# Optimization experiments

Hardware: AMD Instinct MI355X
Metric: run time of the kernel (lower is better)

## Reference

```python
import jax, jax.numpy as jnp
import numpy as np

B, C, H, W = 4, 128, 128, 128
NCLS = 80
NCONV = 2


def conv3x3(x, w, b):
    # x: [B,Cin,H,W], w: [Cout,Cin,3,3]
    y = jax.lax.conv_general_dilated(x, w, (1, 1), 'SAME',
                                     dimension_numbers=('NCHW', 'OIHW', 'NCHW'))
    return y + b[None, :, None, None]


def setup_inputs() -> dict:
    key = jax.random.key(0)
    ks = jax.random.split(key, 10)
    std = 0.01  # conv init std in the torch module
    prior_prob = 0.01
    bias_value = -np.log((1 - prior_prob) / prior_prob)
    inp = {
        'feature': jax.random.normal(ks[0], (B, C, H, W), jnp.float32),
        'targets': jax.random.uniform(ks[1], (B, NCLS, H, W), jnp.float32),
        'cls_w': std * jax.random.normal(ks[2], (NCONV, C, C, 3, 3), jnp.float32),
        'cls_b': jnp.zeros((NCONV, C), jnp.float32),
        'bbox_w': std * jax.random.normal(ks[3], (NCONV, C, C, 3, 3), jnp.float32),
        'bbox_b': jnp.zeros((NCONV, C), jnp.float32),
        'off_w': std * jax.random.normal(ks[4], (NCONV, C, C, 3, 3), jnp.float32),
        'off_b': jnp.zeros((NCONV, C), jnp.float32),
        'cls_score_w': std * jax.random.normal(ks[5], (NCLS, C, 3, 3), jnp.float32),
        'cls_score_b': jnp.full((NCLS,), bias_value, jnp.float32),
        'bbox_pred_w': std * jax.random.normal(ks[6], (2, C, 3, 3), jnp.float32),
        'bbox_pred_b': jnp.zeros((2,), jnp.float32),
        'center_off_w': std * jax.random.normal(ks[7], (2, C, 3, 3), jnp.float32),
        'center_off_b': jnp.zeros((2,), jnp.float32),
        'K': 100,
    }
    return inp


def centernet_forward(feature, targets, cls_w, cls_b, bbox_w, bbox_b, off_w, off_b,
                      cls_score_w, cls_score_b, bbox_pred_w, bbox_pred_b,
                      center_off_w, center_off_b, K):
    # ---- head: three conv+ReLU subnets + final 3x3 heads ----
    xc, xb, xo = feature, feature, feature
    for i in range(NCONV):
        xc = jax.nn.relu(conv3x3(xc, cls_w[i], cls_b[i]))
        xb = jax.nn.relu(conv3x3(xb, bbox_w[i], bbox_b[i]))
        xo = jax.nn.relu(conv3x3(xo, off_w[i], off_b[i]))
    logits = conv3x3(xc, cls_score_w, cls_score_b)      # [B,NCLS,H,W]
    wh = conv3x3(xb, bbox_pred_w, bbox_pred_b)          # [B,2,H,W]
    off = conv3x3(xo, center_off_w, center_off_b)       # [B,2,H,W]

    # ---- center focal loss (alpha=2, beta=4, reduction='sum') ----
    pos = (targets == 1.0).astype(logits.dtype)
    neg = (targets < 1.0).astype(logits.dtype)
    neg_w = jnp.power(1.0 - targets, 4.0)
    p = jax.nn.sigmoid(logits)
    log_p = jax.nn.log_sigmoid(logits)        # log(sigmoid(x))
    log_1mp = jax.nn.log_sigmoid(-logits)     # log(1 - sigmoid(x))
    pos_loss = log_p * jnp.square(1.0 - p) * pos
    neg_loss = log_1mp * jnp.square(p) * neg_w * neg
    loss = -(pos_loss.sum()) - (neg_loss.sum())

    # ---- decode: sigmoid + 3x3 maxpool pseudo-NMS + top-k + gather ----
    hm = p  # sigmoid heatmap
    hmax = jax.lax.reduce_window(hm, -jnp.inf, jax.lax.max,
                                 (1, 1, 3, 3), (1, 1, 1, 1), 'SAME')
    hm_nms = jnp.where(hmax == hm, hm, 0.0)
    scores, inds = jax.lax.top_k(hm_nms.reshape(B, -1), K)  # [B,K]
    hw = H * W
    clses = inds // hw                 # [B,K] int class ids
    sp = inds % hw                     # spatial index
    ys = (sp // W).astype(jnp.float32)
    xs = (sp % W).astype(jnp.float32)
    # gather wh/offset at peak locations
    wh_k = jnp.take_along_axis(wh.reshape(B, 2, hw), sp[:, None, :], axis=2)    # [B,2,K]
    off_k = jnp.take_along_axis(off.reshape(B, 2, hw), sp[:, None, :], axis=2)  # [B,2,K]
    cx = xs + off_k[:, 0]
    cy = ys + off_k[:, 1]
    w_, h_ = wh_k[:, 0], wh_k[:, 1]
    boxes = jnp.stack([cx - w_ / 2, cy - h_ / 2, cx + w_ / 2, cy + h_ / 2], axis=-1)  # [B,K,4]
    return boxes, scores, clses, loss


def reference(feature, targets, cls_w, cls_b, bbox_w, bbox_b, off_w, off_b,
              cls_score_w, cls_score_b, bbox_pred_w, bbox_pred_b,
              center_off_w, center_off_b, K):
    return centernet_forward(feature, targets, cls_w, cls_b, bbox_w, bbox_b,
                             off_w, off_b, cls_score_w, cls_score_b,
                             bbox_pred_w, bbox_pred_b, center_off_w,
                             center_off_b, K)
```

## Files before the change

### kernel.cpp

```cpp
#include <hip/hip_runtime.h>
#include <hip/hip_bf16.h>
#include <math.h>

#define B_    4
#define C_    128
#define H_    128
#define W_    128
#define HW_   (H_*W_)
#define NCLS_ 80
#define KTOP  100
#define CAPB  2048

typedef __attribute__((ext_vector_type(8)))  short bf16x8;
typedef __attribute__((ext_vector_type(16))) float f32x16;

#define WSTAGE_B   18432
#define WIMG_B     663552
#define NIMG       7
#define XROWB      144
#define XCOLS      130
#define XPITCH     (XCOLS * XROWB)
#define XSZ        ((size_t)16 * 130 * XPITCH)
#define XLDS_B     25920
#define LDS_TOT    (XLDS_B + 2 * WSTAGE_B)
#define ZERO_N     20512

__device__ __forceinline__ unsigned bf16_rne(float x) {
    unsigned u = __float_as_uint(x);
    return (u + 0x7FFFu + ((u >> 16) & 1u)) >> 16;
}
__device__ __forceinline__ void split2(float v0, float v1, unsigned& hiP, unsigned& loP) {
    unsigned h0 = bf16_rne(v0), h1 = bf16_rne(v1);
    float r0 = v0 - __uint_as_float(h0 << 16);
    float r1 = v1 - __uint_as_float(h1 << 16);
    unsigned l0 = bf16_rne(r0), l1 = bf16_rne(r1);
    hiP = h0 | (h1 << 16);
    loP = l0 | (l1 << 16);
}

#define MFMA32(a, bvec, c) __builtin_amdgcn_mfma_f32_32x32x16_bf16(a, bvec, c, 0, 0, 0)

__global__ __launch_bounds__(256) void init_k(char* __restrict__ xa, char* __restrict__ xb,
                                              unsigned* __restrict__ sm, float* __restrict__ loss)
{
    const int i = blockIdx.x * 256 + threadIdx.x;
    if (i < 16512) {
        char* buf = (i < 8256) ? xa : xb;
        const int j = (i < 8256) ? i : i - 8256;
        int R, col;
        if (j < 4160) {
            const int g = j / 260, rr = j % 260;
            R = g * 130 + ((rr < 130) ? 0 : 129);
            col = rr % 130;
        } else {
            const int q = j - 4160;
            const int g = q / 256, m = q % 256;
            R = g * 130 + 1 + (m >> 1);
            col = (m & 1) ? 129 : 0;
        }
        char* p = buf + ((size_t)R * XCOLS + col) * XROWB;
        #pragma unroll
        for (int k = 0; k < 9; k++) *(uint4*)(p + k * 16) = make_uint4(0, 0, 0, 0);
    } else {
        const int k = i - 16512;
        if (k < ZERO_N) sm[k] = 0u;
        if (k == ZERO_N) *loss = 0.f;
    }
}

struct WtArgs { const float* src[NIMG]; int cout[NIMG]; };

__global__ __launch_bounds__(256) void wtx_k(WtArgs a, unsigned short* wt)
{
    const int img = blockIdx.z;
    const int idx = blockIdx.x * 256 + threadIdx.x;
    const int cp    = idx & 15;
    const int co    = (idx >> 4) & 127;
    const int st    = idx >> 11;
    if (st >= 36) return;
    const int tap   = st % 9;
    const int chunk = st / 9;
    const float* w = a.src[img];
    const int Cout = a.cout[img];
    const int ci = chunk * 32 + 2 * cp;
    float v0 = 0.f, v1 = 0.f;
    if (co < Cout) {
        v0 = w[((size_t)co * 128 + ci) * 9 + tap];
        v1 = w[((size_t)co * 128 + ci + 1) * 9 + tap];
    }
    unsigned hiP, loP; split2(v0, v1, hiP, loP);
    char* dst = (char*)wt + (size_t)img * WIMG_B + ((size_t)st * 128 + co) * 144;
    *(unsigned*)(dst + 4 * cp)      = hiP;
    *(unsigned*)(dst + 64 + 4 * cp) = loP;
    if (cp < 4) *(unsigned*)(dst + 128 + 4 * cp) = 0u;
}

__device__ __forceinline__ void stage_w(const unsigned short* wt, char* lds,
                                        int s, int buf, int wv, int lane)
{
    const int nc    = (wv < 2) ? 5 : 4;
    const int start = (wv < 2) ? wv * 5 : 10 + (wv - 2) * 4;
    const char* src = (const char*)wt + (size_t)s * WSTAGE_B;
    char* dst = lds + XLDS_B + buf * WSTAGE_B;
    for (int i = 0; i < nc; i++) {
        const int off = (start + i) * 1024;
        __builtin_amdgcn_global_load_lds(
            (const __attribute__((address_space(1))) unsigned*)(src + off + lane * 16),
            (__attribute__((address_space(3))) unsigned*)(dst + off),
            16, 0, 0);
    }
}

template<int RELU, int XOUT>
__device__ __forceinline__ void conv_epilogue(
    f32x16 (&acc)[2][2], const bool* act,
    const float* bias, float* outf, char* outx, int Cout,
    int b, int x0, int y0, int wm, int wn, int kh, int l31)
{
    #pragma unroll
    for (int f = 0; f < 2; f++) {
        if (!act[f]) continue;
        if (XOUT == 0) {
            #pragma unroll
            for (int r = 0; r < 16; r++) {
                const int co = wm * 64 + f * 32 + 4 * kh + (r & 3) + 8 * (r >> 2);
                if (co < Cout) {
                    const float bv = bias[co];
                    #pragma unroll
                    for (int fn = 0; fn < 2; fn++) {
                        const int p = wn * 64 + fn * 32 + l31;
                        float v = acc[f][fn][r] + bv;
                        if (RELU) v = fmaxf(v, 0.f);
                        outf[((size_t)b * Cout + co) * HW_ + (size_t)(y0 + (p >> 4)) * 128 + (x0 + (p & 15))] = v;
                    }
                }
            }
        } else {
            const int chunkO = wm * 2 + f;
            #pragma unroll
            for (int r2 = 0; r2 < 8; r2++) {
                const int r = 2 * r2;
                const int cij = 4 * kh + (r & 3) + 8 * (r >> 2);
                const int co0 = wm * 64 + f * 32 + cij;
                const float b0v = bias[co0], b1v = bias[co0 + 1];
                #pragma unroll
                for (int fn = 0; fn < 2; fn++) {
                    const int p = wn * 64 + fn * 32 + l31;
                    float v0 = acc[f][fn][r] + b0v;
                    float v1 = acc[f][fn][r + 1] + b1v;
                    if (RELU) { v0 = fmaxf(v0, 0.f); v1 = fmaxf(v1, 0.f); }
                    unsigned hiP, loP; split2(v0, v1, hiP, loP);
                    char* rowp = outx + ((size_t)((b * 4 + chunkO) * 130 + (y0 + (p >> 4) + 1)) * XCOLS
                                        + (x0 + (p & 15) + 1)) * XROWB;
                    *(unsigned*)(rowp + 2 * cij)      = hiP;
                    *(unsigned*)(rowp + 64 + 2 * cij) = loP;
                }
            }
        }
    }
}

template<int RELU, int XOUT>
__global__ __launch_bounds__(256, 2) void conv_f_k(
    const float* __restrict__ in, const unsigned short* __restrict__ wt,
    const float* __restrict__ bias, float* __restrict__ outf,
    char* __restrict__ outx, int Cout)
{
    __shared__ __align__(16) char lds[LDS_TOT];

    const int t    = threadIdx.x;
    const int lane = t & 63;
    const int wv   = t >> 6;
    const int wm   = wv >> 1;
    const int wn   = wv & 1;
    const int l31  = lane & 31;
    const int kh   = lane >> 5;

    const int bi = blockIdx.x;
    const int x0 = (bi & 7) << 4;
    const int y0 = ((bi >> 3) & 15) << 3;
    const int b  = bi >> 7;

    int baddr[2];
    #pragma unroll
    for (int fn = 0; fn < 2; fn++) {
        const int p = wn * 64 + fn * 32 + l31;
        baddr[fn] = ((p >> 4) * 18 + (p & 15)) * 144 + kh * 16;
    }
    int aaddr[2];
    bool act[2];
    #pragma unroll
    for (int f = 0; f < 2; f++) {
        aaddr[f] = XLDS_B + (wm * 64 + f * 32 + l31) * 144 + kh * 16;
        act[f] = (wm * 64 + f * 32) < Cout;
    }

    f32x16 acc[2][2];
    #pragma unroll
    for (int i = 0; i < 2; i++)
        #pragma unroll
        for (int j = 0; j < 2; j++)
            #pragma unroll
            for (int r = 0; r < 16; r++) acc[i][j][r] = 0.f;

    const float* inb = in + (size_t)b * 128 * HW_;

    float xa[12], xb[12];
    #define LOADX(ch) do {                                                    \
        _Pragma("unroll")                                                     \
        for (int it = 0; it < 12; it++) {                                     \
            const int idx = t + it * 256;                                     \
            const int pl = idx & 15, cp = (idx >> 4) & 15, ph = idx >> 8;     \
            const int pos = ph * 16 + pl;                                     \
            float v0 = 0.f, v1 = 0.f;                                         \
            if (pos < 180) {                                                  \
                const int hy = pos / 18, hx = pos - hy * 18;                  \
                const int gy = y0 - 1 + hy, gx = x0 - 1 + hx;                 \
                if ((unsigned)gy < 128u && (unsigned)gx < 128u) {             \
                    const float* p0 = inb + (size_t)((ch) * 32 + 2 * cp) * HW_ \
                                          + gy * 128 + gx;                    \
                    v0 = p0[0]; v1 = p0[HW_];                                 \
                }                                                             \
            }                                                                 \
            xa[it] = v0; xb[it] = v1;                                         \
        }                                                                     \
    } while (0)

    stage_w(wt, lds, 0, 0, wv, lane);
    LOADX(0);

    for (int chunk = 0; chunk < 4; chunk++) {
        if (chunk) {
            __builtin_amdgcn_s_barrier();
            __builtin_amdgcn_sched_barrier(0);
        }
        #pragma unroll
        for (int it = 0; it < 12; it++) {
            const int idx = t + it * 256;
            const int pl = idx & 15, cp = (idx >> 4) & 15, ph = idx >> 8;
            const int pos = ph * 16 + pl;
            if (pos < 180) {
                unsigned hiP, loP; split2(xa[it], xb[it], hiP, loP);
                *(unsigned*)(lds + pos * 144 + 4 * cp)      = hiP;
                *(unsigned*)(lds + pos * 144 + 64 + 4 * cp) = loP;
            }
        }
        asm volatile("s_waitcnt vmcnt(0) lgkmcnt(0)" ::: "memory");
        __builtin_amdgcn_s_barrier();
        __builtin_amdgcn_sched_barrier(0);

        #pragma unroll
        for (int tap = 0; tap < 9; tap++) {
            const int s = chunk * 9 + tap;
            if (tap) {
                asm volatile("s_waitcnt vmcnt(0)" ::: "memory");
                __builtin_amdgcn_sched_barrier(0);
                __builtin_amdgcn_s_barrier();
                __builtin_amdgcn_sched_barrier(0);
            }
            if (s + 1 < 36)
                stage_w(wt, lds, s + 1, (s + 1) & 1, wv, lane);
            if (tap == 0 && chunk < 3)
                LOADX(chunk + 1);

            const int wsel = (s & 1) * WSTAGE_B;
            const int doff = ((tap / 3) * 18 + (tap % 3)) * 144;

            #pragma unroll
            for (int ks = 0; ks < 2; ks++) {
                bf16x8 bh[2], bl[2], ah[2], al[2];
                #pragma unroll
                for (int fn = 0; fn < 2; fn++) {
                    bh[fn] = *(const bf16x8*)(lds + baddr[fn] + doff + ks * 32);
                    bl[fn] = *(const bf16x8*)(lds + baddr[fn] + doff + ks * 32 + 64);
                }
                #pragma unroll
                for (int f = 0; f < 2; f++) {
                    ah[f] = *(const bf16x8*)(lds + aaddr[f] + wsel + ks * 32);
                    al[f] = *(const bf16x8*)(lds + aaddr[f] + wsel + ks * 32 + 64);
                }
                #pragma unroll
                for (int f = 0; f < 2; f++)
                    if (act[f])
                        #pragma unroll
                        for (int fn = 0; fn < 2; fn++)
                            acc[f][fn] = MFMA32(ah[f], bh[fn], acc[f][fn]);
                #pragma unroll
                for (int f = 0; f < 2; f++)
                    if (act[f])
                        #pragma unroll
                        for (int fn = 0; fn < 2; fn++)
                            acc[f][fn] = MFMA32(ah[f], bl[fn], acc[f][fn]);
                #pragma unroll
                for (int f = 0; f < 2; f++)
                    if (act[f])
                        #pragma unroll
                        for (int fn = 0; fn < 2; fn++)
                            acc[f][fn] = MFMA32(al[f], bh[fn], acc[f][fn]);
            }
        }
    }
    #undef LOADX
    conv_epilogue<RELU, XOUT>(acc, act, bias, outf, outx, Cout, b, x0, y0, wm, wn, kh, l31);
}

template<int RELU, int XOUT>
__global__ __launch_bounds__(256, 2) void conv_x_k(
    const char* __restrict__ xin, const unsigned short* __restrict__ wt,
    const float* __restrict__ bias, float* __restrict__ outf,
    char* __restrict__ outx, int Cout)
{
    __shared__ __align__(16) char lds[LDS_TOT];

    const int t    = threadIdx.x;
    const int lane = t & 63;
    const int wv   = t >> 6;
    const int wm   = wv >> 1;
    const int wn   = wv & 1;
    const int l31  = lane & 31;
    const int kh   = lane >> 5;

    const int bi = blockIdx.x;
    const int x0 = (bi & 7) << 4;
    const int y0 = ((bi >> 3) & 15) << 3;
    const int b  = bi >> 7;

    int baddr[2];
    #pragma unroll
    for (int fn = 0; fn < 2; fn++) {
        const int p = wn * 64 + fn * 32 + l31;
        baddr[fn] = (p >> 4) * 2592 + (p & 15) * 144 + kh * 16;
    }
    int aaddr[2];
    bool act[2];
    #pragma unroll
    for (int f = 0; f < 2; f++) {
        aaddr[f] = XLDS_B + (wm * 64 + f * 32 + l31) * 144 + kh * 16;
        act[f] = (wm * 64 + f * 32) < Cout;
    }

    f32x16 acc[2][2];
    #pragma unroll
    for (int i = 0; i < 2; i++)
        #pragma unroll
        for (int j = 0; j < 2; j++)
            #pragma unroll
            for (int r = 0; r < 16; r++) acc[i][j][r] = 0.f;

    stage_w(wt, lds, 0, 0, wv, lane);

    for (int chunk = 0; chunk < 4; chunk++) {
        if (chunk) {
            __builtin_amdgcn_s_barrier();
            __builtin_amdgcn_sched_barrier(0);
        }
        const size_t rowbase = ((size_t)((b * 4 + chunk) * 130 + y0) * XCOLS + x0) * XROWB;
        #pragma unroll
        for (int gg = 0; gg < 5; gg++) {
            const int g = wv * 5 + gg;
            const int hy = g >> 1, i = g & 1;
            __builtin_amdgcn_global_load_lds(
                (const __attribute__((address_space(1))) unsigned*)
                    (xin + rowbase + (size_t)hy * XPITCH + i * 1024 + lane * 16),
                (__attribute__((address_space(3))) unsigned*)(lds + hy * 2592 + i * 1024),
                16, 0, 0);
        }
        for (int u = t; u < 340; u += 256) {
            const int hy = u / 34;
            const int off = 2048 + (u % 34) * 16;
            uint4 v = *(const uint4*)(xin + rowbase + (size_t)hy * XPITCH + off);
            *(uint4*)(lds + hy * 2592 + off) = v;
        }
        asm volatile("s_waitcnt vmcnt(0) lgkmcnt(0)" ::: "memory");
        __builtin_amdgcn_s_barrier();
        __builtin_amdgcn_sched_barrier(0);

        #pragma unroll
        for (int tap = 0; tap < 9; tap++) {
            const int s = chunk * 9 + tap;
            if (tap) {
                asm volatile("s_waitcnt vmcnt(0)" ::: "memory");
                __builtin_amdgcn_sched_barrier(0);
                __builtin_amdgcn_s_barrier();
                __builtin_amdgcn_sched_barrier(0);
            }
            if (s + 1 < 36)
                stage_w(wt, lds, s + 1, (s + 1) & 1, wv, lane);

            const int wsel = (s & 1) * WSTAGE_B;
            const int doff = (tap / 3) * 2592 + (tap % 3) * 144;

            #pragma unroll
            for (int ks = 0; ks < 2; ks++) {
                bf16x8 bh[2], bl[2], ah[2], al[2];
                #pragma unroll
                for (int fn = 0; fn < 2; fn++) {
                    bh[fn] = *(const bf16x8*)(lds + baddr[fn] + doff + ks * 32);
                    bl[fn] = *(const bf16x8*)(lds + baddr[fn] + doff + ks * 32 + 64);
                }
                #pragma unroll
                for (int f = 0; f < 2; f++) {
                    ah[f] = *(const bf16x8*)(lds + aaddr[f] + wsel + ks * 32);
                    al[f] = *(const bf16x8*)(lds + aaddr[f] + wsel + ks * 32 + 64);
                }
                #pragma unroll
                for (int f = 0; f < 2; f++)
                    if (act[f])
                        #pragma unroll
                        for (int fn = 0; fn < 2; fn++)
                            acc[f][fn] = MFMA32(ah[f], bh[fn], acc[f][fn]);
                #pragma unroll
                for (int f = 0; f < 2; f++)
                    if (act[f])
                        #pragma unroll
                        for (int fn = 0; fn < 2; fn++)
                            acc[f][fn] = MFMA32(ah[f], bl[fn], acc[f][fn]);
                #pragma unroll
                for (int f = 0; f < 2; f++)
                    if (act[f])
                        #pragma unroll
                        for (int fn = 0; fn < 2; fn++)
                            acc[f][fn] = MFMA32(al[f], bh[fn], acc[f][fn]);
            }
        }
    }
    conv_epilogue<RELU, XOUT>(acc, act, bias, outf, outx, Cout, b, x0, y0, wm, wn, kh, l31);
}

__global__ __launch_bounds__(256) void conv2out_k(
    const float* __restrict__ in, const float* __restrict__ w,
    const float* __restrict__ bias, float* __restrict__ out)
{
    __shared__ float ws[128 * 9 * 2];
    const int t = threadIdx.x;
    for (int i = t; i < 2304; i += 256) {
        const int co = i & 1, tap = (i >> 1) % 9, ci = i / 18;
        ws[i] = w[(size_t)co * 1152 + ci * 9 + tap];
    }
    __syncthreads();

    const int b  = blockIdx.y;
    const int y  = (blockIdx.x >> 3) * 16 + (t >> 4);
    const int x  = (blockIdx.x & 7) * 16 + (t & 15);
    const float* inb = in + (size_t)b * 128 * HW_ + y * 128 + x;

    float a0 = bias[0], a1 = bias[1];
    #pragma unroll 2
    for (int ci = 0; ci < 128; ci++) {
        const float* p  = inb + (size_t)ci * HW_;
        const float* wp = ws + ci * 18;
        #pragma unroll
        for (int tap = 0; tap < 9; tap++) {
            const int dy = tap / 3 - 1, dx = tap % 3 - 1;
            const int yy = y + dy, xx = x + dx;
            float v = 0.f;
            if ((unsigned)yy < 128u && (unsigned)xx < 128u) v = p[dy * 128 + dx];
            a0 = fmaf(v, wp[tap * 2 + 0], a0);
            a1 = fmaf(v, wp[tap * 2 + 1], a1);
        }
    }
    out[((size_t)b * 2 + 0) * HW_ + y * 128 + x] = a0;
    out[((size_t)b * 2 + 1) * HW_ + y * 128 + x] = a1;
}

__global__ __launch_bounds__(256) void lnh_k(
    const float* __restrict__ L, const float* __restrict__ targets,
    float* __restrict__ loss_out, unsigned* __restrict__ keys,
    unsigned* __restrict__ hist)
{
    __shared__ unsigned h[2048];
    for (int j = threadIdx.x; j < 2048; j += 256) h[j] = 0;
    __syncthreads();

    const int per_b = NCLS_ * HW_;
    const int b = blockIdx.y;
    const float* Lb = L + (size_t)b * per_b;
    const float* Tb = targets + (size_t)b * per_b;
    unsigned* kb = keys + (size_t)b * per_b;

    float sum = 0.f;
    for (int i = blockIdx.x * 256 + threadIdx.x; i < per_b; i += gridDim.x * 256) {
        const float x = Lb[i];
        const float t = Tb[i];
        const float e   = expf(-fabsf(x));
        const float inv = 1.f / (1.f + e);
        const float lp  = log1pf(e);
        const bool  xe  = (x >= 0.f);
        const float p   = xe ? inv : e * inv;
        const float lsp = xe ? -lp : (x - lp);
        const float lsn = lsp - x;
        float om = 1.f - t;
        float nw = om * om; nw *= nw;
        const float omp = 1.f - p;
        if (t == 1.0f)     sum -= lsp * omp * omp;
        else if (t < 1.0f) sum -= lsn * p * p * nw;

        const int sp = i & (HW_ - 1);
        const int y = sp >> 7, xq = sp & 127;
        const float* plane = Lb + (i - sp);
        const int ym = (y > 0) ? y - 1 : 0,   yp = (y < 127) ? y + 1 : 127;
        const int xm = (xq > 0) ? xq - 1 : 0, xp = (xq < 127) ? xq + 1 : 127;
        const float* r0 = plane + ym * 128;
        const float* r1 = plane + y  * 128;
        const float* r2 = plane + yp * 128;
        float m = fmaxf(fmaxf(fmaxf(r0[xm], r0[xq]), fmaxf(r0[xp], r1[xm])),
                 fmaxf(fmaxf(x, r1[xp]),
                 fmaxf(fmaxf(r2[xm], r2[xq]), r2[xp])));
        const float em   = expf(-fabsf(m));
        const float invm = 1.f / (1.f + em);
        const float pm   = (m >= 0.f) ? invm : em * invm;
        const unsigned key = (__float_as_uint(p) == __float_as_uint(pm)) ? __float_as_uint(p) : 0u;
        kb[i] = key;
        if (key) atomicAdd(&h[key >> 21], 1u);
    }

    #pragma unroll
    for (int off = 32; off > 0; off >>= 1) sum += __shfl_down(sum, off, 64);
    __shared__ float wsum[4];
    int lane = threadIdx.x & 63, wid = threadIdx.x >> 6;
    if (lane == 0) wsum[wid] = sum;
    __syncthreads();
    if (threadIdx.x == 0)
        atomicAdd(loss_out, wsum[0] + wsum[1] + wsum[2] + wsum[3]);

    unsigned* gh = hist + b * 2048;
    for (int j = threadIdx.x; j < 2048; j += 256) if (h[j]) atomicAdd(&gh[j], h[j]);
}

__global__ void hist2_k(const unsigned* __restrict__ keys, const unsigned* __restrict__ bin1,
                        unsigned* __restrict__ hist)
{
    __shared__ unsigned h[2048];
    for (int j = threadIdx.x; j < 2048; j += blockDim.x) h[j] = 0;
    __syncthreads();
    const int per_b = NCLS_ * HW_;
    const int b = blockIdx.y;
    const unsigned b1 = bin1[b];
    const unsigned* kb = keys + (size_t)b * per_b;
    for (int i = blockIdx.x * blockDim.x + threadIdx.x; i < per_b; i += gridDim.x * blockDim.x) {
        unsigned k = kb[i];
        if (k && (k >> 21) == b1) atomicAdd(&h[(k >> 10) & 2047], 1u);
    }
    __syncthreads();
    unsigned* gh = hist + b * 2048;
    for (int j = threadIdx.x; j < 2048; j += blockDim.x) if (h[j]) atomicAdd(&gh[j], h[j]);
}

__global__ void hist3_k(const unsigned* __restrict__ keys, const unsigned* __restrict__ pfx2,
                        unsigned* __restrict__ hist)
{
    __shared__ unsigned h[1024];
    for (int j = threadIdx.x; j < 1024; j += blockDim.x) h[j] = 0;
    __syncthreads();
    const int per_b = NCLS_ * HW_;
    const int b = blockIdx.y;
    const unsigned p2 = pfx2[b];
    const unsigned* kb = keys + (size_t)b * per_b;
    for (int i = blockIdx.x * blockDim.x + threadIdx.x; i < per_b; i += gridDim.x * blockDim.x) {
        unsigned k = kb[i];
        if (k && (k >> 10) == p2) atomicAdd(&h[k & 1023], 1u);
    }
    __syncthreads();
    unsigned* gh = hist + b * 1024;
    for (int j = threadIdx.x; j < 1024; j += blockDim.x) if (h[j]) atomicAdd(&gh[j], h[j]);
}

template<int NBINS, int LEVEL>
__global__ __launch_bounds__(256) void scan_k(
    const unsigned* __restrict__ hist,
    const unsigned* __restrict__ inPfx, const unsigned* __restrict__ inGt,
    unsigned* __restrict__ outPfx, unsigned* __restrict__ outGt)
{
    constexpr int PER = NBINS / 256;
    const int b = blockIdx.x;
    const int t = threadIdx.x;
    const unsigned* h = hist + b * NBINS;
    const unsigned base = (LEVEL == 1) ? 0u : inGt[b];

    unsigned v[PER];
    unsigned local = 0;
    #pragma unroll
    for (int i = 0; i < PER; i++) { v[i] = h[t * PER + i]; local += v[i]; }

    __shared__ unsigned ps[256];
    ps[t] = local;
    __syncthreads();
    #pragma unroll
    for (int off = 1; off < 256; off <<= 1) {
        unsigned add = (t + off < 256) ? ps[t + off] : 0u;
        __syncthreads();
        ps[t] += add;
        __syncthreads();
    }
    const unsigned sumAbove = (t == 255) ? 0u : ps[t + 1];

    unsigned sfx = sumAbove;
    #pragma unroll
    for (int i = PER - 1; i >= 0; i--) {
        unsigned sfx_next = sfx;
        sfx += v[i];
        bool cond     = (base + sfx      >= KTOP);
        bool condNext = (base + sfx_next >= KTOP);
        if (cond && !condNext) {
            unsigned sel = (unsigned)(t * PER + i);
            unsigned pfx = (LEVEL == 1) ? sel
                         : (LEVEL == 2) ? ((inPfx[b] << 11) | sel)
                                        : ((inPfx[b] << 10) | sel);
            outPfx[b] = pfx;
            outGt[b]  = base + sfx_next;
        }
    }
    if (t == 0 && base + ps[0] < KTOP) {
        unsigned pfx = (LEVEL == 1) ? 0u
                     : (LEVEL == 2) ? (inPfx[b] << 11)
                                    : (inPfx[b] << 10);
        outPfx[b] = pfx;
        outGt[b]  = base + ps[0];
    }
}

__global__ void select_k(const unsigned* __restrict__ keys, const unsigned* __restrict__ Tk,
                         unsigned* cntA, unsigned* cntB,
                         uint2* __restrict__ listA, unsigned* __restrict__ listB)
{
    const int per_b = NCLS_ * HW_;
    const int b = blockIdx.y;
    const unsigned T = Tk[b];
    const unsigned* kb = keys + (size_t)b * per_b;
    for (int i = blockIdx.x * blockDim.x + threadIdx.x; i < per_b; i += gridDim.x * blockDim.x) {
        unsigned k = kb[i];
        if (k > T) {
            unsigned pos = atomicAdd(&cntA[b], 1u);
            if (pos < KTOP) listA[b * KTOP + pos] = make_uint2(k, (unsigned)i);
        } else if (k == T && k != 0u) {
            unsigned pos = atomicAdd(&cntB[b], 1u);
            if (pos < CAPB) listB[b * CAPB + pos] = (unsigned)i;
        }
    }
}

__global__ void finalize_k(const unsigned* __restrict__ cntA, const unsigned* __restrict__ cntB,
                           const uint2* __restrict__ listA, const unsigned* __restrict__ listB,
                           const unsigned* __restrict__ Tk,
                           const float* __restrict__ wh, const float* __restrict__ off,
                           float* __restrict__ out)
{
    __shared__ unsigned sk[KTOP], si[KTOP], ok[KTOP], oi[KTOP];
    const int b = blockIdx.x;
    const int nA = (int)min(cntA[b], (unsigned)KTOP);
    const unsigned T = Tk[b];

    if ((int)threadIdx.x < nA) {
        uint2 e = listA[b * KTOP + threadIdx.x];
        sk[threadIdx.x] = e.x;
        si[threadIdx.x] = e.y;
    }
    __syncthreads();

    if (threadIdx.x == 0) {
        int need = KTOP - nA;
        unsigned nB = min(cntB[b], (unsigned)CAPB);
        long long prev = -1;
        for (int r = 0; r < need; r++) {
            unsigned best = 0xFFFFFFFFu;
            for (unsigned j = 0; j < nB; j++) {
                unsigned idx = listB[b * CAPB + j];
                if ((long long)idx > prev && idx < best) best = idx;
            }
            if (best == 0xFFFFFFFFu) { sk[nA + r] = 0u; si[nA + r] = 0u; }
            else { sk[nA + r] = T; si[nA + r] = best; prev = (long long)best; }
        }
    }
    __syncthreads();

    if (threadIdx.x < KTOP) {
        unsigned kk = sk[threadIdx.x], ii = si[threadIdx.x];
        int rank = 0;
        for (int j = 0; j < KTOP; j++) {
            unsigned kj = sk[j], ij = si[j];
            rank += (kj > kk) || (kj == kk && ij < ii);
        }
        ok[rank] = kk; oi[rank] = ii;
    }
    __syncthreads();

    if (threadIdx.x < KTOP) {
        int r = threadIdx.x;
        unsigned ind = oi[r];
        float score = __uint_as_float(ok[r]);
        int cls = (int)(ind / HW_);
        int sp  = (int)(ind % HW_);
        float ysf = (float)(sp >> 7);
        float xsf = (float)(sp & 127);
        float w0 = wh[((size_t)b * 2 + 0) * HW_ + sp];
        float h0 = wh[((size_t)b * 2 + 1) * HW_ + sp];
        float o0 = off[((size_t)b * 2 + 0) * HW_ + sp];
        float o1 = off[((size_t)b * 2 + 1) * HW_ + sp];
        float cx = xsf + o0;
        float cy = ysf + o1;
        float* boxes  = out;
        float* scores = out + (size_t)B_ * KTOP * 4;
        float* clses  = out + (size_t)B_ * KTOP * 5;
        boxes[((size_t)b * KTOP + r) * 4 + 0] = cx - w0 * 0.5f;
        boxes[((size_t)b * KTOP + r) * 4 + 1] = cy - h0 * 0.5f;
        boxes[((size_t)b * KTOP + r) * 4 + 2] = cx + w0 * 0.5f;
        boxes[((size_t)b * KTOP + r) * 4 + 3] = cy + h0 * 0.5f;
        scores[b * KTOP + r] = score;
        clses[b * KTOP + r]  = (float)cls;
    }
}

extern "C" void kernel_launch(void* const* d_in, const int* in_sizes, int n_in,
                              void* d_out, int out_size, void* d_ws, size_t ws_size,
                              hipStream_t stream)
{
    const float* feature      = (const float*)d_in[0];
    const float* targets      = (const float*)d_in[1];
    const float* cls_w        = (const float*)d_in[2];
    const float* cls_b        = (const float*)d_in[3];
    const float* bbox_w       = (const float*)d_in[4];
    const float* bbox_b       = (const float*)d_in[5];
    const float* off_w        = (const float*)d_in[6];
    const float* off_b        = (const float*)d_in[7];
    const float* cls_score_w  = (const float*)d_in[8];
    const float* cls_score_b  = (const float*)d_in[9];
    const float* bbox_pred_w  = (const float*)d_in[10];
    const float* bbox_pred_b  = (const float*)d_in[11];
    const float* center_off_w = (const float*)d_in[12];
    const float* center_off_b = (const float*)d_in[13];
    float* out = (float*)d_out;

    const size_t L_BYTES  = (size_t)B_ * NCLS_ * HW_ * 4;
    const size_t P_BYTES  = (size_t)B_ * 2 * HW_ * 4;
    const size_t WT_BYTES = (size_t)NIMG * WIMG_B;

    char* ws = (char*)d_ws;
    const size_t lw = (size_t)C_ * C_ * 9;
    float* loss_ptr = out + (size_t)B_ * KTOP * 6;

    char* XA = ws;
    char* XB = ws + XSZ;
    float* L   = (float*)(ws + 2 * XSZ);
    float* WH  = (float*)(ws + 2 * XSZ + L_BYTES);
    float* OFF = (float*)(ws + 2 * XSZ + L_BYTES + P_BYTES);
    unsigned short* WT = (unsigned short*)(ws + 2 * XSZ + L_BYTES + 2 * P_BYTES);
    unsigned* sm = (unsigned*)(ws + 2 * XSZ + L_BYTES + 2 * P_BYTES + WT_BYTES);
    float* Bf = (float*)XB;
    unsigned* keys = (unsigned*)XB;

    unsigned* hist1 = sm;
    unsigned* hist2 = sm + 4 * 2048;
    unsigned* hist3 = sm + 8 * 2048;
    unsigned* bin1  = sm + 8 * 2048 + 4 * 1024;
    unsigned* gt1   = bin1 + 4;
    unsigned* pfx2  = bin1 + 8;
    unsigned* gt2   = bin1 + 12;
    unsigned* Tk    = bin1 + 16;
    unsigned* gt3   = bin1 + 20;
    unsigned* cntA  = bin1 + 24;
    unsigned* cntB  = bin1 + 28;
    uint2*    listA = (uint2*)(bin1 + 32);
    unsigned* listB = (unsigned*)(bin1 + 32 + 2 * B_ * KTOP);

    WtArgs wa;
    wa.src[0] = cls_w;        wa.cout[0] = 128;
    wa.src[1] = bbox_w;       wa.cout[1] = 128;
    wa.src[2] = off_w;        wa.cout[2] = 128;
    wa.src[3] = cls_w + lw;   wa.cout[3] = 128;
    wa.src[4] = bbox_w + lw;  wa.cout[4] = 128;
    wa.src[5] = off_w + lw;   wa.cout[5] = 128;
    wa.src[6] = cls_score_w;  wa.cout[6] = NCLS_;

    init_k<<<145, 256, 0, stream>>>(XA, XB, sm, loss_ptr);
    wtx_k<<<dim3(288, 1, NIMG), 256, 0, stream>>>(wa, WT);

    #define WIMG(i) (WT + (size_t)(i) * (WIMG_B / 2))

    conv_f_k<1, 1><<<512, 256, 0, stream>>>(feature, WIMG(0), cls_b,       nullptr, XA, 128);
    conv_x_k<1, 1><<<512, 256, 0, stream>>>(XA,      WIMG(3), cls_b + C_,  nullptr, XB, 128);
    conv_x_k<0, 0><<<512, 256, 0, stream>>>(XB,      WIMG(6), cls_score_b, L, nullptr, NCLS_);
    conv_f_k<1, 1><<<512, 256, 0, stream>>>(feature, WIMG(1), bbox_b,      nullptr, XA, 128);
    conv_x_k<1, 0><<<512, 256, 0, stream>>>(XA,      WIMG(4), bbox_b + C_, Bf, nullptr, 128);
    conv2out_k<<<dim3(64, 4), 256, 0, stream>>>(Bf, bbox_pred_w, bbox_pred_b, WH);
    conv_f_k<1, 1><<<512, 256, 0, stream>>>(feature, WIMG(2), off_b,       nullptr, XA, 128);
    conv_x_k<1, 0><<<512, 256, 0, stream>>>(XA,      WIMG(5), off_b + C_,  Bf, nullptr, 128);
    conv2out_k<<<dim3(64, 4), 256, 0, stream>>>(Bf, center_off_w, center_off_b, OFF);

    lnh_k<<<dim3(512, B_), 256, 0, stream>>>(L, targets, loss_ptr, keys, hist1);

    dim3 hgrid(512, B_);
    scan_k<2048, 1><<<B_, 256, 0, stream>>>(hist1, nullptr, nullptr, bin1, gt1);
    hist2_k<<<hgrid, 256, 0, stream>>>(keys, bin1, hist2);
    scan_k<2048, 2><<<B_, 256, 0, stream>>>(hist2, bin1, gt1, pfx2, gt2);
    hist3_k<<<hgrid, 256, 0, stream>>>(keys, pfx2, hist3);
    scan_k<1024, 3><<<B_, 256, 0, stream>>>(hist3, pfx2, gt2, Tk, gt3);
    select_k<<<hgrid, 256, 0, stream>>>(keys, Tk, cntA, cntB, listA, listB);

    finalize_k<<<B_, 128, 0, stream>>>(cntA, cntB, listA, listB, Tk, WH, OFF, out);
}
```

Baseline: 601.0 us.

## Load MFMA weight fragments directly from global and double-buffer input tiles in LDS

The weight pre-transform now writes weights pre-swizzled into the per-lane MFMA fragment layout, so the conv kernels read A operands straight from global/L2 instead of staging each tap's weights through LDS. This drops the per-tap barriers and LDS weight copies. The freed LDS holds a second activation buffer, so the next input-channel chunk is prefetched during compute with one barrier per chunk. In exchange, weight reads now go through global memory and may add latency and cache pressure on every tap.

New measurement: 619.1 us. +3.0%, slower.

```diff
diff --git a/kernel.cpp b/kernel.cpp
--- a/kernel.cpp
+++ b/kernel.cpp
@@ -14,15 +14,15 @@
 typedef __attribute__((ext_vector_type(8)))  short bf16x8;
 typedef __attribute__((ext_vector_type(16))) float f32x16;
 
-#define WSTAGE_B   18432
-#define WIMG_B     663552
+#define WSTG_B     16384
+#define WIMG_B     589824
 #define NIMG       7
 #define XROWB      144
 #define XCOLS      130
 #define XPITCH     (XCOLS * XROWB)
 #define XSZ        ((size_t)16 * 130 * XPITCH)
 #define XLDS_B     25920
-#define LDS_TOT    (XLDS_B + 2 * WSTAGE_B)
+#define LDS_TOT    (2 * XLDS_B)
 #define ZERO_N     20512
 
 __device__ __forceinline__ unsigned bf16_rne(float x) {
@@ -74,41 +74,28 @@
 {
     const int img = blockIdx.z;
     const int idx = blockIdx.x * 256 + threadIdx.x;
-    const int cp    = idx & 15;
-    const int co    = (idx >> 4) & 127;
-    const int st    = idx >> 11;
+    const int h  = idx & 1;
+    const int ks = (idx >> 1) & 1;
+    const int r  = (idx >> 2) & 31;
+    const int g  = (idx >> 7) & 3;
+    const int st = idx >> 9;
     if (st >= 36) return;
-    const int tap   = st % 9;
-    const int chunk = st / 9;
+    const int tap = st % 9, chunk = st / 9;
     const float* w = a.src[img];
     const int Cout = a.cout[img];
-    const int ci = chunk * 32 + 2 * cp;
-    float v0 = 0.f, v1 = 0.f;
-    if (co < Cout) {
-        v0 = w[((size_t)co * 128 + ci) * 9 + tap];
-        v1 = w[((size_t)co * 128 + ci + 1) * 9 + tap];
-    }
-    unsigned hiP, loP; split2(v0, v1, hiP, loP);
-    char* dst = (char*)wt + (size_t)img * WIMG_B + ((size_t)st * 128 + co) * 144;
-    *(unsigned*)(dst + 4 * cp)      = hiP;
-    *(unsigned*)(dst + 64 + 4 * cp) = loP;
-    if (cp < 4) *(unsigned*)(dst + 128 + 4 * cp) = 0u;
-}
-
-__device__ __forceinline__ void stage_w(const unsigned short* wt, char* lds,
-                                        int s, int buf, int wv, int lane)
-{
-    const int nc    = (wv < 2) ? 5 : 4;
-    const int start = (wv < 2) ? wv * 5 : 10 + (wv - 2) * 4;
-    const char* src = (const char*)wt + (size_t)s * WSTAGE_B;
-    char* dst = lds + XLDS_B + buf * WSTAGE_B;
-    for (int i = 0; i < nc; i++) {
-        const int off = (start + i) * 1024;
-        __builtin_amdgcn_global_load_lds(
-            (const __attribute__((address_space(1))) unsigned*)(src + off + lane * 16),
-            (__attribute__((address_space(3))) unsigned*)(dst + off),
-            16, 0, 0);
-    }
+    const int cout = g * 32 + r;
+    const int cin0 = chunk * 32 + ks * 16 + h * 8;
+    float v[8];
+    #pragma unroll
+    for (int j = 0; j < 8; j++)
+        v[j] = (cout < Cout) ? w[((size_t)cout * 128 + cin0 + j) * 9 + tap] : 0.f;
+    unsigned hiW[4], loW[4];
+    #pragma unroll
+    for (int j = 0; j < 4; j++) split2(v[2 * j], v[2 * j + 1], hiW[j], loW[j]);
+    char* dst = (char*)wt + (size_t)img * WIMG_B + (size_t)st * WSTG_B
+              + g * 4096 + ks * 2048 + r * 32 + h * 16;
+    *(uint4*)dst          = make_uint4(hiW[0], hiW[1], hiW[2], hiW[3]);
+    *(uint4*)(dst + 1024) = make_uint4(loW[0], loW[1], loW[2], loW[3]);
 }
 
 template<int RELU, int XOUT>
@@ -187,13 +174,12 @@
         const int p = wn * 64 + fn * 32 + l31;
         baddr[fn] = ((p >> 4) * 18 + (p & 15)) * 144 + kh * 16;
     }
-    int aaddr[2];
     bool act[2];
     #pragma unroll
-    for (int f = 0; f < 2; f++) {
-        aaddr[f] = XLDS_B + (wm * 64 + f * 32 + l31) * 144 + kh * 16;
-        act[f] = (wm * 64 + f * 32) < Cout;
-    }
+    for (int f = 0; f < 2; f++) act[f] = (wm * 64 + f * 32) < Cout;
+
+    const int wlane = ((lane & 31) << 5) | (kh << 4);
+    const char* wb = (const char*)wt + wm * 8192 + wlane;
 
     f32x16 acc[2][2];
     #pragma unroll
@@ -226,49 +212,48 @@
         }                                                                     \
     } while (0)
 
-    stage_w(wt, lds, 0, 0, wv, lane);
+    #define STOREX(bufsel) do {                                               \
+        _Pragma("unroll")                                                     \
+        for (int it = 0; it < 12; it++) {                                     \
+            const int idx = t + it * 256;                                     \
+            const int pl = idx & 15, cp = (idx >> 4) & 15, ph = idx >> 8;     \
+            const int pos = ph * 16 + pl;                                     \
+            if (pos < 180) {                                                  \
+                unsigned hiP, loP; split2(xa[it], xb[it], hiP, loP);          \
+                *(unsigned*)(lds + (bufsel) * XLDS_B + pos * 144 + 4 * cp)      = hiP; \
+                *(unsigned*)(lds + (bufsel) * XLDS_B + pos * 144 + 64 + 4 * cp) = loP; \
+            }                                                                 \
+        }                                                                     \
+    } while (0)
+
     LOADX(0);
+    STOREX(0);
+    __syncthreads();
 
     for (int chunk = 0; chunk < 4; chunk++) {
-        if (chunk) {
-            __builtin_amdgcn_s_barrier();
-            __builtin_amdgcn_sched_barrier(0);
-        }
-        #pragma unroll
-        for (int it = 0; it < 12; it++) {
-            const int idx = t + it * 256;
-            const int pl = idx & 15, cp = (idx >> 4) & 15, ph = idx >> 8;
-            const int pos = ph * 16 + pl;
-            if (pos < 180) {
-                unsigned hiP, loP; split2(xa[it], xb[it], hiP, loP);
-                *(unsigned*)(lds + pos * 144 + 4 * cp)      = hiP;
-                *(unsigned*)(lds + pos * 144 + 64 + 4 * cp) = loP;
-            }
-        }
-        asm volatile("s_waitcnt vmcnt(0) lgkmcnt(0)" ::: "memory");
-        __builtin_amdgcn_s_barrier();
-        __builtin_amdgcn_sched_barrier(0);
+        const int xsel = (chunk & 1) * XLDS_B;
+        if (chunk < 3) LOADX(chunk + 1);
 
         #pragma unroll
         for (int tap = 0; tap < 9; tap++) {
             const int s = chunk * 9 + tap;
-            if (tap) {
-                asm volatile("s_waitcnt vmcnt(0)" ::: "memory");
-                __builtin_amdgcn_sched_barrier(0);
-                __builtin_amdgcn_s_barrier();
-                __builtin_amdgcn_sched_barrier(0);
-            }
-            if (s + 1 < 36)
-                stage_w(wt, lds, s + 1, (s + 1) & 1, wv, lane);
-            if (tap == 0 && chunk < 3)
-                LOADX(chunk + 1);
-
-            const int wsel = (s & 1) * WSTAGE_B;
-            const int doff = ((tap / 3) * 18 + (tap % 3)) * 144;
+            const char* wp = wb + (size_t)s * WSTG_B;
+            bf16x8 ah[2][2], al[2][2];
+            #pragma unroll
+            for (int f = 0; f < 2; f++) {
+                if (act[f]) {
+                    #pragma unroll
+                    for (int ks = 0; ks < 2; ks++) {
+                        ah[f][ks] = *(const bf16x8*)(wp + f * 4096 + ks * 2048);
+                        al[f][ks] = *(const bf16x8*)(wp + f * 4096 + ks * 2048 + 1024);
+                    }
+                }
+            }
+            const int doff = ((tap / 3) * 18 + (tap % 3)) * 144 + xsel;
 
             #pragma unroll
             for (int ks = 0; ks < 2; ks++) {
-                bf16x8 bh[2], bl[2], ah[2], al[2];
+                bf16x8 bh[2], bl[2];
                 #pragma unroll
                 for (int fn = 0; fn < 2; fn++) {
                     bh[fn] = *(const bf16x8*)(lds + baddr[fn] + doff + ks * 32);
@@ -276,31 +261,38 @@
                 }
                 #pragma unroll
                 for (int f = 0; f < 2; f++) {
-                    ah[f] = *(const bf16x8*)(lds + aaddr[f] + wsel + ks * 32);
-                    al[f] = *(const bf16x8*)(lds + aaddr[f] + wsel + ks * 32 + 64);
-                }
-                #pragma unroll
-                for (int f = 0; f < 2; f++)
-                    if (act[f])
+                    if (act[f]) {
                         #pragma unroll
                         for (int fn = 0; fn < 2; fn++)
-                            acc[f][fn] = MFMA32(ah[f], bh[fn], acc[f][fn]);
+                            acc[f][fn] = MFMA32(ah[f][ks], bh[fn], acc[f][fn]);
+                    }
+                }
                 #pragma unroll
-                for (int f = 0; f < 2; f++)
-                    if (act[f])
+                for (int f = 0; f < 2; f++) {
+                    if (act[f]) {
                         #pragma unroll
                         for (int fn = 0; fn < 2; fn++)
-                            acc[f][fn] = MFMA32(ah[f], bl[fn], acc[f][fn]);
+                            acc[f][fn] = MFMA32(ah[f][ks], bl[fn], acc[f][fn]);
+                    }
+                }
                 #pragma unroll
-                for (int f = 0; f < 2; f++)
-                    if (act[f])
+                for (int f = 0; f < 2; f++) {
+                    if (act[f]) {
                         #pragma unroll
                         for (int fn = 0; fn < 2; fn++)
-                            acc[f][fn] = MFMA32(al[f], bh[fn], acc[f][fn]);
-            }
+                            acc[f][fn] = MFMA32(al[f][ks], bh[fn], acc[f][fn]);
+                    }
+                }
+            }
+        }
+
+        if (chunk < 3) {
+            STOREX((chunk + 1) & 1);
+            __syncthreads();
         }
     }
     #undef LOADX
+    #undef STOREX
     conv_epilogue<RELU, XOUT>(acc, act, bias, outf, outx, Cout, b, x0, y0, wm, wn, kh, l31);
 }
 
@@ -331,13 +323,12 @@
         const int p = wn * 64 + fn * 32 + l31;
         baddr[fn] = (p >> 4) * 2592 + (p & 15) * 144 + kh * 16;
     }
-    int aaddr[2];
     bool act[2];
     #pragma unroll
-    for (int f = 0; f < 2; f++) {
-        aaddr[f] = XLDS_B + (wm * 64 + f * 32 + l31) * 144 + kh * 16;
-        act[f] = (wm * 64 + f * 32) < Cout;
-    }
+    for (int f = 0; f < 2; f++) act[f] = (wm * 64 + f * 32) < Cout;
+
+    const int wlane = ((lane & 31) << 5) | (kh << 4);
+    const char* wb = (const char*)wt + wm * 8192 + wlane;
 
     f32x16 acc[2][2];
     #pragma unroll
@@ -347,14 +338,8 @@
             #pragma unroll
             for (int r = 0; r < 16; r++) acc[i][j][r] = 0.f;
 
-    stage_w(wt, lds, 0, 0, wv, lane);
-
-    for (int chunk = 0; chunk < 4; chunk++) {
-        if (chunk) {
-            __builtin_amdgcn_s_barrier();
-            __builtin_amdgcn_sched_barrier(0);
-        }
-        const size_t rowbase = ((size_t)((b * 4 + chunk) * 130 + y0) * XCOLS + x0) * XROWB;
+    {
+        const size_t rowbase = ((size_t)((b * 4 + 0) * 130 + y0) * XCOLS + x0) * XROWB;
         #pragma unroll
         for (int gg = 0; gg < 5; gg++) {
             const int g = wv * 5 + gg;
@@ -371,28 +356,62 @@
             uint4 v = *(const uint4*)(xin + rowbase + (size_t)hy * XPITCH + off);
             *(uint4*)(lds + hy * 2592 + off) = v;
         }
-        asm volatile("s_waitcnt vmcnt(0) lgkmcnt(0)" ::: "memory");
-        __builtin_amdgcn_s_barrier();
-        __builtin_amdgcn_sched_barrier(0);
+    }
+    __syncthreads();
+
+    for (int chunk = 0; chunk < 4; chunk++) {
+        const int xsel = (chunk & 1) * XLDS_B;
+
+        uint4 tl0, tl1;
+        bool h0 = false, h1 = false;
+        int xd = 0;
+        size_t rowb1 = 0;
+        if (chunk < 3) {
+            xd    = ((chunk + 1) & 1) * XLDS_B;
+            rowb1 = ((size_t)((b * 4 + chunk + 1) * 130 + y0) * XCOLS + x0) * XROWB;
+            #pragma unroll
+            for (int gg = 0; gg < 5; gg++) {
+                const int g = wv * 5 + gg;
+                const int hy = g >> 1, i = g & 1;
+                __builtin_amdgcn_global_load_lds(
+                    (const __attribute__((address_space(1))) unsigned*)
+                        (xin + rowb1 + (size_t)hy * XPITCH + i * 1024 + lane * 16),
+                    (__attribute__((address_space(3))) unsigned*)(lds + xd + hy * 2592 + i * 1024),
+                    16, 0, 0);
+            }
+            h0 = (t < 340);
+            h1 = (t < 84);
+            if (h0) {
+                const int hy = t / 34, off = 2048 + (t % 34) * 16;
+                tl0 = *(const uint4*)(xin + rowb1 + (size_t)hy * XPITCH + off);
+            }
+            if (h1) {
+                const int u = t + 256;
+                const int hy = u / 34, off = 2048 + (u % 34) * 16;
+                tl1 = *(const uint4*)(xin + rowb1 + (size_t)hy * XPITCH + off);
+            }
+        }
 
         #pragma unroll
         for (int tap = 0; tap < 9; tap++) {
             const int s = chunk * 9 + tap;
-            if (tap) {
-                asm volatile("s_waitcnt vmcnt(0)" ::: "memory");
-                __builtin_amdgcn_sched_barrier(0);
-                __builtin_amdgcn_s_barrier();
-                __builtin_amdgcn_sched_barrier(0);
-            }
-            if (s + 1 < 36)
-                stage_w(wt, lds, s + 1, (s + 1) & 1, wv, lane);
-
-            const int wsel = (s & 1) * WSTAGE_B;
-            const int doff = (tap / 3) * 2592 + (tap % 3) * 144;
+            const char* wp = wb + (size_t)s * WSTG_B;
+            bf16x8 ah[2][2], al[2][2];
+            #pragma unroll
+            for (int f = 0; f < 2; f++) {
+                if (act[f]) {
+                    #pragma unroll
+                    for (int ks = 0; ks < 2; ks++) {
+                        ah[f][ks] = *(const bf16x8*)(wp + f * 4096 + ks * 2048);
+                        al[f][ks] = *(const bf16x8*)(wp + f * 4096 + ks * 2048 + 1024);
+                    }
+                }
+            }
+            const int doff = (tap / 3) * 2592 + (tap % 3) * 144 + xsel;
 
             #pragma unroll
             for (int ks = 0; ks < 2; ks++) {
-                bf16x8 bh[2], bl[2], ah[2], al[2];
+                bf16x8 bh[2], bl[2];
                 #pragma unroll
                 for (int fn = 0; fn < 2; fn++) {
                     bh[fn] = *(const bf16x8*)(lds + baddr[fn] + doff + ks * 32);
@@ -400,28 +419,42 @@
                 }
                 #pragma unroll
                 for (int f = 0; f < 2; f++) {
-                    ah[f] = *(const bf16x8*)(lds + aaddr[f] + wsel + ks * 32);
-                    al[f] = *(const bf16x8*)(lds + aaddr[f] + wsel + ks * 32 + 64);
-                }
-                #pragma unroll
-                for (int f = 0; f < 2; f++)
-                    if (act[f])
+                    if (act[f]) {
                         #pragma unroll
                         for (int fn = 0; fn < 2; fn++)
-                            acc[f][fn] = MFMA32(ah[f], bh[fn], acc[f][fn]);
+                            acc[f][fn] = MFMA32(ah[f][ks], bh[fn], acc[f][fn]);
+                    }
+                }
                 #pragma unroll
-                for (int f = 0; f < 2; f++)
-                    if (act[f])
+                for (int f = 0; f < 2; f++) {
+                    if (act[f]) {
                         #pragma unroll
                         for (int fn = 0; fn < 2; fn++)
-                            acc[f][fn] = MFMA32(ah[f], bl[fn], acc[f][fn]);
+                            acc[f][fn] = MFMA32(ah[f][ks], bl[fn], acc[f][fn]);
+                    }
+                }
                 #pragma unroll
-                for (int f = 0; f < 2; f++)
-                    if (act[f])
+                for (int f = 0; f < 2; f++) {
+                    if (act[f]) {
                         #pragma unroll
                         for (int fn = 0; fn < 2; fn++)
-                            acc[f][fn] = MFMA32(al[f], bh[fn], acc[f][fn]);
-            }
+                            acc[f][fn] = MFMA32(al[f][ks], bh[fn], acc[f][fn]);
+                    }
+                }
+            }
+        }
+
+        if (chunk < 3) {
+            if (h0) {
+                const int hy = t / 34, off = 2048 + (t % 34) * 16;
+                *(uint4*)(lds + xd + hy * 2592 + off) = tl0;
+            }
+            if (h1) {
+                const int u = t + 256;
+                const int hy = u / 34, off = 2048 + (u % 34) * 16;
+                *(uint4*)(lds + xd + hy * 2592 + off) = tl1;
+            }
+            __syncthreads();
         }
     }
     conv_epilogue<RELU, XOUT>(acc, act, bias, outf, outx, Cout, b, x0, y0, wm, wn, kh, l31);
@@ -772,7 +805,7 @@
     wa.src[6] = cls_score_w;  wa.cout[6] = NCLS_;
 
     init_k<<<145, 256, 0, stream>>>(XA, XB, sm, loss_ptr);
-    wtx_k<<<dim3(288, 1, NIMG), 256, 0, stream>>>(wa, WT);
+    wtx_k<<<dim3(72, 1, NIMG), 256, 0, stream>>>(wa, WT);
 
     #define WIMG(i) (WT + (size_t)(i) * (WIMG_B / 2))
 
```
